# Kernel tuning notes

Hardware: AMD Instinct MI355X
Metric: run time of the kernel (lower is better)

## Reference

```python
import jax, jax.numpy as jnp
import numpy as np

ALPHA = 0.3
D_K = 64


def setup_inputs() -> dict:
    key = jax.random.key(0)
    kq, kk, kv = jax.random.split(key, 3)
    B, H, S, D = 4, 16, 2048, 64
    Q = jax.random.normal(kq, (B, H, S, D), dtype=jnp.float32)
    K = jax.random.normal(kk, (B, H, S, D), dtype=jnp.float32)
    V = jax.random.normal(kv, (B, H, S, D), dtype=jnp.float32)
    attn_mask = jnp.zeros((B, H, S, S), dtype=bool)
    return {"Q": Q, "K": K, "V": V, "attn_mask": attn_mask}


def reference(Q, K, V, attn_mask):
    # scores: [B,H,S,S] = QK^T / sqrt(d_k)
    scores = jnp.einsum("bhqd,bhkd->bhqk", Q, K) / np.sqrt(D_K).astype(np.float32)
    # adj_tanh(x, a) = (e^{ax}-e^{-ax})/(e^{ax}+e^{-ax}) == tanh(a*x)
    attn = jnp.tanh(ALPHA * scores)
    # NOTE: original torch code calls attn.masked_fill(...) (non in-place) and
    # discards the result, so the mask has NO effect on the output. Replicated
    # faithfully: attn_mask is accepted but unused.
    context = jnp.einsum("bhqk,bhkd->bhqd", attn, V)
    return context
```

## Files before the change

### kernel.cpp

```cpp
#include <hip/hip_runtime.h>


constexpr int S_LEN = 2048;
constexpr int DIM   = 64;
constexpr int QT    = 256;
constexpr int KT    = 64;

constexpr float C_EXP2 = 0.10820212528f;

typedef __bf16 bf16_t;
typedef bf16_t bf16x4 __attribute__((ext_vector_type(4)));
typedef bf16_t bf16x8 __attribute__((ext_vector_type(8)));
typedef float  f32x4  __attribute__((ext_vector_type(4)));

__device__ inline bf16x8 to_bf8(float4 a, float4 b) {
    bf16x8 v;
    v[0] = (bf16_t)a.x; v[1] = (bf16_t)a.y; v[2] = (bf16_t)a.z; v[3] = (bf16_t)a.w;
    v[4] = (bf16_t)b.x; v[5] = (bf16_t)b.y; v[6] = (bf16_t)b.z; v[7] = (bf16_t)b.w;
    return v;
}

__global__ __launch_bounds__(512, 4) void tanh_attn_kernel(
    const float* __restrict__ Q, const float* __restrict__ K,
    const float* __restrict__ V, float* __restrict__ O)
{
    const int tid  = threadIdx.x;
    const int lane = tid & 63;
    const int wv   = tid >> 6;
    const int lr   = lane & 15;
    const int lg   = lane >> 4;

    const int nwg = gridDim.x;
    const int bid = (blockIdx.x & 7) * (nwg >> 3) + (blockIdx.x >> 3);
    const int qtile = bid & 7;
    const int bh    = bid >> 3;
    const int base  = bh * (S_LEN * DIM);
    const int q0    = qtile * QT;

    __shared__ bf16_t Ql[QT * DIM];
    __shared__ bf16_t Kl[KT * DIM];
    __shared__ bf16_t Vt[DIM * KT];

    #pragma unroll
    for (int it = 0; it < 4; ++it) {
        int cid = tid + it * 512;
        int r   = cid >> 3;
        int c8  = (cid & 7) * 8;
        const float* src = Q + base + (q0 + r) * DIM + c8;
        float4 a = *(const float4*)src;
        float4 b = *(const float4*)(src + 4);
        *(bf16x8*)&Ql[r * DIM + (c8 ^ ((r & 7) << 3))] = to_bf8(a, b);
    }
    __syncthreads();

    bf16x8 qa[2][2];
    #pragma unroll
    for (int rt = 0; rt < 2; ++rt)
        #pragma unroll
        for (int ks = 0; ks < 2; ++ks) {
            int r = wv * 32 + rt * 16 + lr;
            int c = ks * 32 + lg * 8;
            qa[rt][ks] = *(const bf16x8*)&Ql[r * DIM + (c ^ ((r & 7) << 3))];
        }
    __syncthreads();

    f32x4 oacc[2][4] = {};

    bf16_t* Pl = Ql + wv * (32 * KT);

    for (int kt = 0; kt < S_LEN / KT; ++kt) {
        const int k0 = kt * KT;

        {
            int r   = tid >> 3;
            int c8  = (tid & 7) * 8;
            const float* src = K + base + (k0 + r) * DIM + c8;
            float4 a = *(const float4*)src;
            float4 b = *(const float4*)(src + 4);
            *(bf16x8*)&Kl[r * DIM + (c8 ^ ((r & 7) << 3))] = to_bf8(a, b);
        }
        {
            int d   = tid & 63;
            int kv0 = (tid >> 6) * 8;
            const float* src = V + base + (k0 + kv0) * DIM + d;
            bf16x8 v;
            #pragma unroll
            for (int j = 0; j < 8; ++j) v[j] = (bf16_t)src[j * DIM];
            *(bf16x8*)&Vt[d * KT + (kv0 ^ ((d & 7) << 3))] = v;
        }
        __syncthreads();

        f32x4 sacc[2][4] = {};
        #pragma unroll
        for (int ct = 0; ct < 4; ++ct) {
            int r = ct * 16 + lr;
            bf16x8 kb0 = *(const bf16x8*)&Kl[r * DIM + ((lg * 8)      ^ ((r & 7) << 3))];
            bf16x8 kb1 = *(const bf16x8*)&Kl[r * DIM + ((32 + lg * 8) ^ ((r & 7) << 3))];
            #pragma unroll
            for (int rt = 0; rt < 2; ++rt) {
                sacc[rt][ct] = __builtin_amdgcn_mfma_f32_16x16x32_bf16(kb0, qa[rt][0], sacc[rt][ct], 0, 0, 0);
                sacc[rt][ct] = __builtin_amdgcn_mfma_f32_16x16x32_bf16(kb1, qa[rt][1], sacc[rt][ct], 0, 0, 0);
            }
        }

        #pragma unroll
        for (int rt = 0; rt < 2; ++rt)
            #pragma unroll
            for (int ct = 0; ct < 4; ++ct) {
                bf16x4 p4;
                #pragma unroll
                for (int j = 0; j < 4; ++j) {
                    float t = __builtin_amdgcn_exp2f(sacc[rt][ct][j] * C_EXP2);
                    p4[j] = (bf16_t)(1.0f - 2.0f * __builtin_amdgcn_rcpf(t + 1.0f));
                }
                int q  = rt * 16 + lr;
                int c0 = ct * 16 + lg * 4;
                *(bf16x4*)&Pl[q * KT + (c0 ^ ((q & 7) << 3))] = p4;
            }

        bf16x8 pa[2][2];
        #pragma unroll
        for (int rt = 0; rt < 2; ++rt)
            #pragma unroll
            for (int ks = 0; ks < 2; ++ks) {
                int r = rt * 16 + lr;
                pa[rt][ks] = *(const bf16x8*)&Pl[r * KT + ((ks * 32 + lg * 8) ^ ((r & 7) << 3))];
            }

        #pragma unroll
        for (int dt = 0; dt < 4; ++dt) {
            int d = dt * 16 + lr;
            bf16x8 vb0 = *(const bf16x8*)&Vt[d * KT + ((lg * 8)      ^ ((d & 7) << 3))];
            bf16x8 vb1 = *(const bf16x8*)&Vt[d * KT + ((32 + lg * 8) ^ ((d & 7) << 3))];
            #pragma unroll
            for (int rt = 0; rt < 2; ++rt) {
                oacc[rt][dt] = __builtin_amdgcn_mfma_f32_16x16x32_bf16(pa[rt][0], vb0, oacc[rt][dt], 0, 0, 0);
                oacc[rt][dt] = __builtin_amdgcn_mfma_f32_16x16x32_bf16(pa[rt][1], vb1, oacc[rt][dt], 0, 0, 0);
            }
        }
        __syncthreads();
    }

    #pragma unroll
    for (int rt = 0; rt < 2; ++rt)
        #pragma unroll
        for (int dt = 0; dt < 4; ++dt)
            #pragma unroll
            for (int j = 0; j < 4; ++j) {
                int q = q0 + wv * 32 + rt * 16 + lg * 4 + j;
                int d = dt * 16 + lr;
                O[base + q * DIM + d] = oacc[rt][dt][j];
            }
}

extern "C" void kernel_launch(void* const* d_in, const int* in_sizes, int n_in,
                              void* d_out, int out_size, void* d_ws, size_t ws_size,
                              hipStream_t stream) {
    const float* Q = (const float*)d_in[0];
    const float* K = (const float*)d_in[1];
    const float* V = (const float*)d_in[2];
    float* O = (float*)d_out;
    dim3 grid(64 * (S_LEN / QT));
    dim3 block(512);
    hipLaunchKernelGGL(tanh_attn_kernel, grid, block, 0, stream, Q, K, V, O);
}
```

Before: 109.6 us.

## Double-buffer K/V tiles with register prefetch and MFMA priority hints

K and V tiles are now double-buffered in shared memory. Global loads for the next tile go into registers at the start of each iteration and are converted and stored into the other buffer after the PV matmul, so memory latency overlaps with compute and one barrier per iteration is removed. s_setprio is raised around the MFMA sections to favour matrix issue across waves. The cost is extra LDS (two K and two V tiles) and live registers for the prefetched data, which may reduce occupancy under the 512x4 launch bounds.

Result: faster. 104.8 us (-4.4%).

```diff
diff --git a/kernel.cpp b/kernel.cpp
--- a/kernel.cpp
+++ b/kernel.cpp
@@ -5,6 +5,7 @@
 constexpr int DIM   = 64;
 constexpr int QT    = 256;
 constexpr int KT    = 64;
+constexpr int NKT   = S_LEN / KT;
 
 constexpr float C_EXP2 = 0.10820212528f;
 
@@ -38,8 +39,27 @@
     const int q0    = qtile * QT;
 
     __shared__ bf16_t Ql[QT * DIM];
-    __shared__ bf16_t Kl[KT * DIM];
-    __shared__ bf16_t Vt[DIM * KT];
+    __shared__ bf16_t Kl[2][KT * DIM];
+    __shared__ bf16_t Vt[2][DIM * KT];
+
+    const float* Kb = K + base;
+    const float* Vb = V + base;
+
+    const int sr  = tid >> 3;
+    const int sc8 = (tid & 7) * 8;
+    const int sd  = tid & 63;
+    const int skv = (tid >> 6) * 8;
+
+    float4 ka, kb2;
+    float  vv[8];
+    {
+        const float* src = Kb + sr * DIM + sc8;
+        ka  = *(const float4*)src;
+        kb2 = *(const float4*)(src + 4);
+        const float* vsrc = Vb + skv * DIM + sd;
+        #pragma unroll
+        for (int j = 0; j < 8; ++j) vv[j] = vsrc[j * DIM];
+    }
 
     #pragma unroll
     for (int it = 0; it < 4; ++it) {
@@ -62,46 +82,51 @@
             int c = ks * 32 + lg * 8;
             qa[rt][ks] = *(const bf16x8*)&Ql[r * DIM + (c ^ ((r & 7) << 3))];
         }
-    __syncthreads();
+
+    {
+        *(bf16x8*)&Kl[0][sr * DIM + (sc8 ^ ((sr & 7) << 3))] = to_bf8(ka, kb2);
+        bf16x8 v;
+        #pragma unroll
+        for (int j = 0; j < 8; ++j) v[j] = (bf16_t)vv[j];
+        *(bf16x8*)&Vt[0][sd * KT + (skv ^ ((sd & 7) << 3))] = v;
+    }
 
     f32x4 oacc[2][4] = {};
-
     bf16_t* Pl = Ql + wv * (32 * KT);
 
-    for (int kt = 0; kt < S_LEN / KT; ++kt) {
-        const int k0 = kt * KT;
-
-        {
-            int r   = tid >> 3;
-            int c8  = (tid & 7) * 8;
-            const float* src = K + base + (k0 + r) * DIM + c8;
-            float4 a = *(const float4*)src;
-            float4 b = *(const float4*)(src + 4);
-            *(bf16x8*)&Kl[r * DIM + (c8 ^ ((r & 7) << 3))] = to_bf8(a, b);
-        }
-        {
-            int d   = tid & 63;
-            int kv0 = (tid >> 6) * 8;
-            const float* src = V + base + (k0 + kv0) * DIM + d;
-            bf16x8 v;
-            #pragma unroll
-            for (int j = 0; j < 8; ++j) v[j] = (bf16_t)src[j * DIM];
-            *(bf16x8*)&Vt[d * KT + (kv0 ^ ((d & 7) << 3))] = v;
-        }
+    #pragma unroll 2
+    for (int kt = 0; kt < NKT; ++kt) {
+        const int cur = kt & 1;
+
         __syncthreads();
 
+        if (kt + 1 < NKT) {
+            const int k0n = (kt + 1) * KT;
+            const float* src = Kb + (k0n + sr) * DIM + sc8;
+            ka  = *(const float4*)src;
+            kb2 = *(const float4*)(src + 4);
+            const float* vsrc = Vb + (k0n + skv) * DIM + sd;
+            #pragma unroll
+            for (int j = 0; j < 8; ++j) vv[j] = vsrc[j * DIM];
+        }
+
+        const bf16_t* Kc = Kl[cur];
+        const bf16_t* Vc = Vt[cur];
+
         f32x4 sacc[2][4] = {};
+        __builtin_amdgcn_s_setprio(1);
         #pragma unroll
         for (int ct = 0; ct < 4; ++ct) {
             int r = ct * 16 + lr;
-            bf16x8 kb0 = *(const bf16x8*)&Kl[r * DIM + ((lg * 8)      ^ ((r & 7) << 3))];
-            bf16x8 kb1 = *(const bf16x8*)&Kl[r * DIM + ((32 + lg * 8) ^ ((r & 7) << 3))];
+            bf16x8 kf0 = *(const bf16x8*)&Kc[r * DIM + ((lg * 8)      ^ ((r & 7) << 3))];
+            bf16x8 kf1 = *(const bf16x8*)&Kc[r * DIM + ((32 + lg * 8) ^ ((r & 7) << 3))];
             #pragma unroll
             for (int rt = 0; rt < 2; ++rt) {
-                sacc[rt][ct] = __builtin_amdgcn_mfma_f32_16x16x32_bf16(kb0, qa[rt][0], sacc[rt][ct], 0, 0, 0);
-                sacc[rt][ct] = __builtin_amdgcn_mfma_f32_16x16x32_bf16(kb1, qa[rt][1], sacc[rt][ct], 0, 0, 0);
-            }
-        }
+                sacc[rt][ct] = __builtin_amdgcn_mfma_f32_16x16x32_bf16(kf0, qa[rt][0], sacc[rt][ct], 0, 0, 0);
+                sacc[rt][ct] = __builtin_amdgcn_mfma_f32_16x16x32_bf16(kf1, qa[rt][1], sacc[rt][ct], 0, 0, 0);
+            }
+        }
+        __builtin_amdgcn_s_setprio(0);
 
         #pragma unroll
         for (int rt = 0; rt < 2; ++rt)
@@ -127,18 +152,28 @@
                 pa[rt][ks] = *(const bf16x8*)&Pl[r * KT + ((ks * 32 + lg * 8) ^ ((r & 7) << 3))];
             }
 
+        __builtin_amdgcn_s_setprio(1);
         #pragma unroll
         for (int dt = 0; dt < 4; ++dt) {
             int d = dt * 16 + lr;
-            bf16x8 vb0 = *(const bf16x8*)&Vt[d * KT + ((lg * 8)      ^ ((d & 7) << 3))];
-            bf16x8 vb1 = *(const bf16x8*)&Vt[d * KT + ((32 + lg * 8) ^ ((d & 7) << 3))];
+            bf16x8 vf0 = *(const bf16x8*)&Vc[d * KT + ((lg * 8)      ^ ((d & 7) << 3))];
+            bf16x8 vf1 = *(const bf16x8*)&Vc[d * KT + ((32 + lg * 8) ^ ((d & 7) << 3))];
             #pragma unroll
             for (int rt = 0; rt < 2; ++rt) {
-                oacc[rt][dt] = __builtin_amdgcn_mfma_f32_16x16x32_bf16(pa[rt][0], vb0, oacc[rt][dt], 0, 0, 0);
-                oacc[rt][dt] = __builtin_amdgcn_mfma_f32_16x16x32_bf16(pa[rt][1], vb1, oacc[rt][dt], 0, 0, 0);
-            }
-        }
-        __syncthreads();
+                oacc[rt][dt] = __builtin_amdgcn_mfma_f32_16x16x32_bf16(pa[rt][0], vf0, oacc[rt][dt], 0, 0, 0);
+                oacc[rt][dt] = __builtin_amdgcn_mfma_f32_16x16x32_bf16(pa[rt][1], vf1, oacc[rt][dt], 0, 0, 0);
+            }
+        }
+        __builtin_amdgcn_s_setprio(0);
+
+        if (kt + 1 < NKT) {
+            const int nxt = cur ^ 1;
+            *(bf16x8*)&Kl[nxt][sr * DIM + (sc8 ^ ((sr & 7) << 3))] = to_bf8(ka, kb2);
+            bf16x8 v;
+            #pragma unroll
+            for (int j = 0; j < 8; ++j) v[j] = (bf16_t)vv[j];
+            *(bf16x8*)&Vt[nxt][sd * KT + (skv ^ ((sd & 7) << 3))] = v;
+        }
     }
 
     #pragma unroll
```
